# Optimization experiments

Measured on AMD Instinct MI355X. Metric: run time of the kernel, lower is better.

Reference implementation:

```python
import jax, jax.numpy as jnp
import numpy as np

CH = 512   # ch_in = c_out
P = 8
SD = 512
NG = CH // P          # n_groups = 64
CIG = CH // NG        # c_in per group = 8
DN = ('NCHW', 'OIHW', 'NCHW')


def setup_inputs() -> dict:
    key = jax.random.key(0)
    ks = jax.random.split(key, 8)
    N, H, W = 8, 128, 128
    return {
        "style_encoding": jax.random.normal(ks[0], (N, SD, 4, 4), jnp.float32),
        "predicted": jax.random.normal(ks[1], (N, CH, H, W), jnp.float32),
        "dw_w": jax.random.normal(ks[2], (CH * CIG, SD, 2, 2), jnp.float32) * 0.02,
        "dw_b": jnp.zeros((CH * CIG,), jnp.float32),
        "pk_w": jax.random.normal(ks[3], (CH * CIG, SD), jnp.float32) * 0.02,
        "pk_b": jnp.zeros((CH * CIG,), jnp.float32),
        "pb_w": jax.random.normal(ks[4], (CH, SD), jnp.float32) * 0.02,
        "pb_b": jnp.zeros((CH,), jnp.float32),
    }


def reference(style_encoding, predicted, dw_w, dw_b, pk_w, pk_b, pb_w, pb_b):
    N, ch, h, w = predicted.shape
    # --- KernelPredictor ---
    # depthwise kernels: 2x2 conv on 4x4 style -> 3x3 spatial kernels
    dw = jax.lax.conv_general_dilated(style_encoding, dw_w, (1, 1), 'VALID',
                                      dimension_numbers=DN)
    dw = dw + dw_b[None, :, None, None]
    depthwise = dw.reshape(N, CH, CIG, 3, 3)
    # avg-pool 4x4 -> (N, SD); 1x1 convs become matmuls
    s_pool = style_encoding.mean(axis=(2, 3))
    pw_kn = (s_pool @ pk_w.T + pk_b).reshape(N, CH, CH // NG)
    pw_bias = s_pool @ pb_w.T + pb_b  # (N, CH)
    # --- instance norm (calc_mean_std, unbiased var, eps=1e-5) ---
    mean = predicted.mean(axis=(2, 3), keepdims=True)
    std = jnp.sqrt(predicted.var(axis=(2, 3), keepdims=True, ddof=1) + 1e-5)
    x = (predicted - mean) / std
    # --- reflect pad + per-sample grouped convs, batched as groups ---
    x = jnp.pad(x, ((0, 0), (0, 0), (1, 1), (1, 1)), mode='reflect')
    xb = x.reshape(1, N * ch, h + 2, w + 2)
    wb = depthwise.reshape(N * CH, CIG, 3, 3)
    depth = jax.lax.conv_general_dilated(xb, wb, (1, 1), 'VALID',
                                         dimension_numbers=DN,
                                         feature_group_count=N * NG)
    wp = pw_kn.reshape(N * CH, CH // NG, 1, 1)
    out = jax.lax.conv_general_dilated(depth, wp, (1, 1), 'VALID',
                                       dimension_numbers=DN,
                                       feature_group_count=N * NG)
    out = out + pw_bias.reshape(1, N * CH, 1, 1)
    return out.reshape(N, ch, h, w)
```

## Files before the change

### kernel.cpp

```cpp
#include <hip/hip_runtime.h>

#define N_    8
#define CH_   512
#define SD_   512
#define CIG_  8
#define NG_   64
#define H_    128
#define W_    128
#define HW_   16384
#define KDW   2048
#define NP_   72
#define OC_   4096

#define WS_B     0
#define WS_SPOOL (WS_B + NP_ * KDW)
#define WS_PWKN  (WS_SPOOL + N_ * SD_)
#define WS_PWB   (WS_PWKN + N_ * OC_)
#define WS_DW    (WS_PWB + N_ * CH_)
#define WS_E     (WS_DW + N_ * OC_ * 9)
#define WS_MEAN  (WS_E + N_ * OC_ * 9)
#define WS_RSTD  (WS_MEAN + N_ * CH_)

__global__ __launch_bounds__(256) void prep(const float* __restrict__ style,
                                            float* __restrict__ B,
                                            float* __restrict__ spool,
                                            float* __restrict__ dwacc) {
  const int idx = blockIdx.x * 256 + threadIdx.x;
  const int NB = NP_ * KDW;
  const int NS = N_ * SD_;
  const int NZ = N_ * OC_ * 9;
  if (idx < NB) {
    const int np = idx >> 11;
    const int k = idx & 2047;
    const int n = np / 9, p = np % 9;
    const int py = p / 3, px = p % 3;
    const int ci = k >> 2, uv = k & 3;
    const int u = uv >> 1, v = uv & 1;
    B[idx] = style[(n * SD_ + ci) * 16 + (py + u) * 4 + (px + v)];
  } else if (idx < NB + NS) {
    const int j = idx - NB;
    const float* s = style + j * 16;
    float a = 0.f;
#pragma unroll
    for (int t = 0; t < 16; t++) a += s[t];
    spool[j] = a * (1.0f / 16.0f);
  } else if (idx < NB + NS + NZ) {
    dwacc[idx - NB - NS] = 0.0f;
  }
}

__global__ __launch_bounds__(256) void stats(const float* __restrict__ pred,
                                             float* __restrict__ meanv,
                                             float* __restrict__ rstdv) {
  const int nc = blockIdx.x;
  const float4* p = (const float4*)(pred + (size_t)nc * HW_);
  float s = 0.f, s2 = 0.f;
#pragma unroll
  for (int i = 0; i < 16; i++) {
    const float4 v = p[threadIdx.x + 256 * i];
    s += v.x + v.y + v.z + v.w;
    s2 += v.x * v.x + v.y * v.y + v.z * v.z + v.w * v.w;
  }
  for (int off = 32; off > 0; off >>= 1) {
    s += __shfl_down(s, off, 64);
    s2 += __shfl_down(s2, off, 64);
  }
  __shared__ float as[4], as2[4];
  const int wv = threadIdx.x >> 6;
  if ((threadIdx.x & 63) == 0) { as[wv] = s; as2[wv] = s2; }
  __syncthreads();
  if (threadIdx.x == 0) {
    const float S = as[0] + as[1] + as[2] + as[3];
    const float S2 = as2[0] + as2[1] + as2[2] + as2[3];
    const float mean = S * (1.0f / HW_);
    const float var = (S2 - S * mean) * (1.0f / (HW_ - 1));
    meanv[nc] = mean;
    rstdv[nc] = 1.0f / sqrtf(var + 1e-5f);
  }
}

__global__ __launch_bounds__(256) void pw_gemm(const float* __restrict__ spool,
                                               const float* __restrict__ pkw,
                                               const float* __restrict__ pkb,
                                               const float* __restrict__ pbw,
                                               const float* __restrict__ pbb,
                                               float* __restrict__ pwkn,
                                               float* __restrict__ pwbias) {
  __shared__ float sp[N_ * SD_];
  for (int i = threadIdx.x; i < N_ * SD_; i += 256) sp[i] = spool[i];
  __syncthreads();
  const int col = blockIdx.x * 256 + threadIdx.x;
  const float* w;
  float bias;
  if (col < OC_) { w = pkw + (size_t)col * SD_; bias = pkb[col]; }
  else           { w = pbw + (size_t)(col - OC_) * SD_; bias = pbb[col - OC_]; }
  float acc[8];
#pragma unroll
  for (int nn = 0; nn < 8; nn++) acc[nn] = 0.f;
  for (int k = 0; k < SD_; k += 4) {
    const float4 wv = *(const float4*)(w + k);
#pragma unroll
    for (int nn = 0; nn < 8; nn++) {
      const float4 sv = *(const float4*)(&sp[nn * SD_ + k]);
      acc[nn] = fmaf(wv.x, sv.x, acc[nn]);
      acc[nn] = fmaf(wv.y, sv.y, acc[nn]);
      acc[nn] = fmaf(wv.z, sv.z, acc[nn]);
      acc[nn] = fmaf(wv.w, sv.w, acc[nn]);
    }
  }
  if (col < OC_) {
#pragma unroll
    for (int nn = 0; nn < 8; nn++) pwkn[nn * OC_ + col] = acc[nn] + bias;
  } else {
#pragma unroll
    for (int nn = 0; nn < 8; nn++) pwbias[nn * CH_ + (col - OC_)] = acc[nn] + bias;
  }
}

__global__ __launch_bounds__(256) void dw_gemm(const float* __restrict__ Bg,
                                               const float* __restrict__ Wg,
                                               float* __restrict__ dwacc) {
  __shared__ float Wl[64 * 129];
  const int t = threadIdx.x;
  const int co0 = blockIdx.x * 128;
  const int kbase = blockIdx.y * 256;
  const int co = t & 127;
  const int npb = __builtin_amdgcn_readfirstlane((t >> 7) * 36);
  float acc[36];
#pragma unroll
  for (int j = 0; j < 36; j++) acc[j] = 0.f;

  for (int kc = 0; kc < 256; kc += 64) {
    __syncthreads();
    {
      const int kq = (t & 15) * 4;
      const int cob = t >> 4;
#pragma unroll
      for (int r = 0; r < 8; r++) {
        const int c = cob + r * 16;
        const float4 wv =
            *(const float4*)(Wg + (size_t)(co0 + c) * KDW + kbase + kc + kq);
        Wl[(kq + 0) * 129 + c] = wv.x;
        Wl[(kq + 1) * 129 + c] = wv.y;
        Wl[(kq + 2) * 129 + c] = wv.z;
        Wl[(kq + 3) * 129 + c] = wv.w;
      }
    }
    __syncthreads();
    const float* Bp = Bg + kbase + kc;
    for (int k = 0; k < 64; k += 4) {
      const float w0 = Wl[(k + 0) * 129 + co];
      const float w1 = Wl[(k + 1) * 129 + co];
      const float w2 = Wl[(k + 2) * 129 + co];
      const float w3 = Wl[(k + 3) * 129 + co];
#pragma unroll
      for (int j = 0; j < 36; j++) {
        const float4 b = *(const float4*)(Bp + (npb + j) * KDW + k);
        float a = acc[j];
        a = fmaf(w0, b.x, a);
        a = fmaf(w1, b.y, a);
        a = fmaf(w2, b.z, a);
        a = fmaf(w3, b.w, a);
        acc[j] = a;
      }
    }
  }
#pragma unroll
  for (int j = 0; j < 36; j++) {
    const int np = npb + j;
    const int n = np / 9, p = np % 9;
    atomicAdd(dwacc + (size_t)(n * OC_ + co0 + co) * 9 + p, acc[j]);
  }
}

__global__ __launch_bounds__(256) void eff_k(const float* __restrict__ dwacc,
                                             const float* __restrict__ dwb,
                                             const float* __restrict__ pwkn,
                                             float* __restrict__ Eg) {
  const int idx = blockIdx.x * 256 + threadIdx.x;
  const int co = idx & 7;
  int tmp = idx >> 3;
  const int p = tmp % 9;
  tmp /= 9;
  const int ci = tmp & 7;
  tmp >>= 3;
  const int gc = tmp & 63;
  const int n = tmp >> 6;
  const int c = gc * 8 + co;
  float a = 0.f;
#pragma unroll
  for (int j = 0; j < 8; j++) {
    const int ch = (gc * 8 + j) * 8 + ci;
    a = fmaf(pwkn[n * OC_ + c * 8 + j],
             dwacc[(size_t)(n * OC_ + ch) * 9 + p] + dwb[ch], a);
  }
  Eg[idx] = a;
}

#define ROWS 16
__global__ __launch_bounds__(256) void main_conv(const float* __restrict__ pred,
                                                 const float* __restrict__ Eg,
                                                 const float* __restrict__ pwb,
                                                 const float* __restrict__ meanv,
                                                 const float* __restrict__ rstdv,
                                                 float* __restrict__ out) {
  __shared__ float xl[8 * 18 * 132];
  __shared__ float El[8 * 9 * 8];
  __shared__ float cm[8], cr[8];
  const int t = threadIdx.x;
  const int yt = blockIdx.x;
  const int gc = blockIdx.y;
  const int n = blockIdx.z;
  const int chbase = n * CH_ + gc * 8;

  if (t < 8) {
    cm[t] = meanv[chbase + t];
    cr[t] = rstdv[chbase + t];
  }
  for (int i = t; i < 576; i += 256)
    El[i] = Eg[(size_t)(n * 64 + gc) * 576 + i];
  __syncthreads();

  const int y0 = yt * ROWS;
  for (int i = t; i < 8 * 18 * 130; i += 256) {
    const int col = i % 130;
    const int rr = (i / 130) % 18;
    const int ci = i / (130 * 18);
    int gy = y0 + rr - 1;
    gy = gy < 0 ? -gy : (gy > 127 ? 254 - gy : gy);
    int gx = col - 1;
    gx = gx < 0 ? -gx : (gx > 127 ? 254 - gx : gx);
    const float v = pred[((size_t)(chbase + ci) * 128 + gy) * 128 + gx];
    xl[(ci * 18 + rr) * 132 + col] = (v - cm[ci]) * cr[ci];
  }
  __syncthreads();

  const int y = t >> 4;
  const int xb = (t & 15) * 8;
  float acc[8][8];
#pragma unroll
  for (int co = 0; co < 8; co++)
#pragma unroll
    for (int px = 0; px < 8; px++) acc[co][px] = 0.f;

#pragma unroll 1
  for (int ci = 0; ci < 8; ci++) {
#pragma unroll
    for (int ky = 0; ky < 3; ky++) {
      const float* xr = &xl[(ci * 18 + y + ky) * 132 + xb];
      const float4 xa = *(const float4*)(xr);
      const float4 xc = *(const float4*)(xr + 4);
      const float xw[10] = {xa.x, xa.y, xa.z, xa.w, xc.x,
                            xc.y, xc.z, xc.w, xr[8], xr[9]};
#pragma unroll
      for (int kx = 0; kx < 3; kx++) {
        const float4 e0 = *(const float4*)(&El[(ci * 9 + ky * 3 + kx) * 8]);
        const float4 e1 = *(const float4*)(&El[(ci * 9 + ky * 3 + kx) * 8 + 4]);
        const float ev[8] = {e0.x, e0.y, e0.z, e0.w, e1.x, e1.y, e1.z, e1.w};
#pragma unroll
        for (int co = 0; co < 8; co++)
#pragma unroll
          for (int px = 0; px < 8; px++)
            acc[co][px] = fmaf(ev[co], xw[kx + px], acc[co][px]);
      }
    }
  }

  const int gy = y0 + y;
#pragma unroll
  for (int co = 0; co < 8; co++) {
    const float b = pwb[chbase + co];
    float* op = out + ((size_t)(chbase + co) * 128 + gy) * 128 + xb;
    float4 o0, o1;
    o0.x = acc[co][0] + b; o0.y = acc[co][1] + b;
    o0.z = acc[co][2] + b; o0.w = acc[co][3] + b;
    o1.x = acc[co][4] + b; o1.y = acc[co][5] + b;
    o1.z = acc[co][6] + b; o1.w = acc[co][7] + b;
    *(float4*)op = o0;
    *(float4*)(op + 4) = o1;
  }
}

extern "C" void kernel_launch(void* const* d_in, const int* in_sizes, int n_in,
                              void* d_out, int out_size, void* d_ws,
                              size_t ws_size, hipStream_t stream) {
  const float* style = (const float*)d_in[0];
  const float* pred = (const float*)d_in[1];
  const float* dww = (const float*)d_in[2];
  const float* dwb = (const float*)d_in[3];
  const float* pkw = (const float*)d_in[4];
  const float* pkb = (const float*)d_in[5];
  const float* pbw = (const float*)d_in[6];
  const float* pbb = (const float*)d_in[7];
  float* out = (float*)d_out;
  float* ws = (float*)d_ws;

  float* B = ws + WS_B;
  float* spool = ws + WS_SPOOL;
  float* pwkn = ws + WS_PWKN;
  float* pwbias = ws + WS_PWB;
  float* dwacc = ws + WS_DW;
  float* Eg = ws + WS_E;
  float* meanv = ws + WS_MEAN;
  float* rstdv = ws + WS_RSTD;

  prep<<<dim3(1744), dim3(256), 0, stream>>>(style, B, spool, dwacc);
  stats<<<dim3(4096), dim3(256), 0, stream>>>(pred, meanv, rstdv);
  pw_gemm<<<dim3(18), dim3(256), 0, stream>>>(spool, pkw, pkb, pbw, pbb, pwkn,
                                              pwbias);
  dw_gemm<<<dim3(32, 8), dim3(256), 0, stream>>>(B, dww, dwacc);
  eff_k<<<dim3(1152), dim3(256), 0, stream>>>(dwacc, dwb, pwkn, Eg);
  main_conv<<<dim3(8, 64, 8), dim3(256), 0, stream>>>(pred, Eg, pwbias, meanv,
                                                      rstdv, out);
}
```

Baseline: 975.5 us.

## Split-K small GEMMs with atomics and halve main_conv LDS tile for occupancy

The pw_gemm is split four ways along K, with results accumulated by atomicAdd into zeroed buffers, and the prep kernel is extended to zero those buffers. The dw_gemm split-K factor is doubled so more blocks run in parallel. main_conv now stages input channels in two halves of four, halving its shared-memory tile, and sets launch bounds to allow four blocks per CU, trading an extra barrier and reload phase for occupancy. Atomic accumulation makes the floating-point summation order nondeterministic.

```diff
diff --git a/kernel.cpp b/kernel.cpp
--- a/kernel.cpp
+++ b/kernel.cpp
@@ -21,14 +21,15 @@
 #define WS_MEAN  (WS_E + N_ * OC_ * 9)
 #define WS_RSTD  (WS_MEAN + N_ * CH_)
 
+#define NZERO (N_ * OC_ + N_ * CH_ + N_ * OC_ * 9)
+
 __global__ __launch_bounds__(256) void prep(const float* __restrict__ style,
                                             float* __restrict__ B,
                                             float* __restrict__ spool,
-                                            float* __restrict__ dwacc) {
+                                            float* __restrict__ zbase) {
   const int idx = blockIdx.x * 256 + threadIdx.x;
   const int NB = NP_ * KDW;
   const int NS = N_ * SD_;
-  const int NZ = N_ * OC_ * 9;
   if (idx < NB) {
     const int np = idx >> 11;
     const int k = idx & 2047;
@@ -44,8 +45,8 @@
 #pragma unroll
     for (int t = 0; t < 16; t++) a += s[t];
     spool[j] = a * (1.0f / 16.0f);
-  } else if (idx < NB + NS + NZ) {
-    dwacc[idx - NB - NS] = 0.0f;
+  } else if (idx < NB + NS + NZERO) {
+    zbase[idx - NB - NS] = 0.0f;
   }
 }
 
@@ -86,34 +87,41 @@
                                                const float* __restrict__ pbb,
                                                float* __restrict__ pwkn,
                                                float* __restrict__ pwbias) {
-  __shared__ float sp[N_ * SD_];
-  for (int i = threadIdx.x; i < N_ * SD_; i += 256) sp[i] = spool[i];
+  __shared__ float sp[N_ * 128];
+  const int kb = blockIdx.y * 128;
+  for (int i = threadIdx.x; i < N_ * 128; i += 256) {
+    const int nn = i >> 7, kk = i & 127;
+    sp[i] = spool[nn * SD_ + kb + kk];
+  }
   __syncthreads();
   const int col = blockIdx.x * 256 + threadIdx.x;
   const float* w;
   float bias;
-  if (col < OC_) { w = pkw + (size_t)col * SD_; bias = pkb[col]; }
-  else           { w = pbw + (size_t)(col - OC_) * SD_; bias = pbb[col - OC_]; }
+  if (col < OC_) { w = pkw + (size_t)col * SD_ + kb; bias = pkb[col]; }
+  else           { w = pbw + (size_t)(col - OC_) * SD_ + kb; bias = pbb[col - OC_]; }
   float acc[8];
 #pragma unroll
   for (int nn = 0; nn < 8; nn++) acc[nn] = 0.f;
-  for (int k = 0; k < SD_; k += 4) {
+  for (int k = 0; k < 128; k += 4) {
     const float4 wv = *(const float4*)(w + k);
 #pragma unroll
     for (int nn = 0; nn < 8; nn++) {
-      const float4 sv = *(const float4*)(&sp[nn * SD_ + k]);
+      const float4 sv = *(const float4*)(&sp[nn * 128 + k]);
       acc[nn] = fmaf(wv.x, sv.x, acc[nn]);
       acc[nn] = fmaf(wv.y, sv.y, acc[nn]);
       acc[nn] = fmaf(wv.z, sv.z, acc[nn]);
       acc[nn] = fmaf(wv.w, sv.w, acc[nn]);
     }
   }
+  const float badd = (blockIdx.y == 0) ? bias : 0.0f;
   if (col < OC_) {
 #pragma unroll
-    for (int nn = 0; nn < 8; nn++) pwkn[nn * OC_ + col] = acc[nn] + bias;
+    for (int nn = 0; nn < 8; nn++)
+      atomicAdd(&pwkn[nn * OC_ + col], acc[nn] + badd);
   } else {
 #pragma unroll
-    for (int nn = 0; nn < 8; nn++) pwbias[nn * CH_ + (col - OC_)] = acc[nn] + bias;
+    for (int nn = 0; nn < 8; nn++)
+      atomicAdd(&pwbias[nn * CH_ + (col - OC_)], acc[nn] + badd);
   }
 }
 
@@ -123,14 +131,14 @@
   __shared__ float Wl[64 * 129];
   const int t = threadIdx.x;
   const int co0 = blockIdx.x * 128;
-  const int kbase = blockIdx.y * 256;
+  const int kbase = blockIdx.y * 128;
   const int co = t & 127;
   const int npb = __builtin_amdgcn_readfirstlane((t >> 7) * 36);
   float acc[36];
 #pragma unroll
   for (int j = 0; j < 36; j++) acc[j] = 0.f;
 
-  for (int kc = 0; kc < 256; kc += 64) {
+  for (int kc = 0; kc < 128; kc += 64) {
     __syncthreads();
     {
       const int kq = (t & 15) * 4;
@@ -198,13 +206,11 @@
 }
 
 #define ROWS 16
-__global__ __launch_bounds__(256) void main_conv(const float* __restrict__ pred,
-                                                 const float* __restrict__ Eg,
-                                                 const float* __restrict__ pwb,
-                                                 const float* __restrict__ meanv,
-                                                 const float* __restrict__ rstdv,
-                                                 float* __restrict__ out) {
-  __shared__ float xl[8 * 18 * 132];
+__global__ __launch_bounds__(256, 4) void main_conv(
+    const float* __restrict__ pred, const float* __restrict__ Eg,
+    const float* __restrict__ pwb, const float* __restrict__ meanv,
+    const float* __restrict__ rstdv, float* __restrict__ out) {
+  __shared__ float xl[4 * 18 * 132];
   __shared__ float El[8 * 9 * 8];
   __shared__ float cm[8], cr[8];
   const int t = threadIdx.x;
@@ -222,19 +228,6 @@
   __syncthreads();
 
   const int y0 = yt * ROWS;
-  for (int i = t; i < 8 * 18 * 130; i += 256) {
-    const int col = i % 130;
-    const int rr = (i / 130) % 18;
-    const int ci = i / (130 * 18);
-    int gy = y0 + rr - 1;
-    gy = gy < 0 ? -gy : (gy > 127 ? 254 - gy : gy);
-    int gx = col - 1;
-    gx = gx < 0 ? -gx : (gx > 127 ? 254 - gx : gx);
-    const float v = pred[((size_t)(chbase + ci) * 128 + gy) * 128 + gx];
-    xl[(ci * 18 + rr) * 132 + col] = (v - cm[ci]) * cr[ci];
-  }
-  __syncthreads();
-
   const int y = t >> 4;
   const int xb = (t & 15) * 8;
   float acc[8][8];
@@ -244,24 +237,45 @@
     for (int px = 0; px < 8; px++) acc[co][px] = 0.f;
 
 #pragma unroll 1
-  for (int ci = 0; ci < 8; ci++) {
-#pragma unroll
-    for (int ky = 0; ky < 3; ky++) {
-      const float* xr = &xl[(ci * 18 + y + ky) * 132 + xb];
-      const float4 xa = *(const float4*)(xr);
-      const float4 xc = *(const float4*)(xr + 4);
-      const float xw[10] = {xa.x, xa.y, xa.z, xa.w, xc.x,
-                            xc.y, xc.z, xc.w, xr[8], xr[9]};
-#pragma unroll
-      for (int kx = 0; kx < 3; kx++) {
-        const float4 e0 = *(const float4*)(&El[(ci * 9 + ky * 3 + kx) * 8]);
-        const float4 e1 = *(const float4*)(&El[(ci * 9 + ky * 3 + kx) * 8 + 4]);
-        const float ev[8] = {e0.x, e0.y, e0.z, e0.w, e1.x, e1.y, e1.z, e1.w};
-#pragma unroll
-        for (int co = 0; co < 8; co++)
-#pragma unroll
-          for (int px = 0; px < 8; px++)
-            acc[co][px] = fmaf(ev[co], xw[kx + px], acc[co][px]);
+  for (int half = 0; half < 2; half++) {
+    if (half) __syncthreads();
+    for (int i = t; i < 4 * 18 * 130; i += 256) {
+      const int col = i % 130;
+      const int rr = (i / 130) % 18;
+      const int cl = i / (130 * 18);
+      const int ci = half * 4 + cl;
+      int gy = y0 + rr - 1;
+      gy = gy < 0 ? -gy : (gy > 127 ? 254 - gy : gy);
+      int gx = col - 1;
+      gx = gx < 0 ? -gx : (gx > 127 ? 254 - gx : gx);
+      const float v = pred[((size_t)(chbase + ci) * 128 + gy) * 128 + gx];
+      xl[(cl * 18 + rr) * 132 + col] = (v - cm[ci]) * cr[ci];
+    }
+    __syncthreads();
+
+#pragma unroll 1
+    for (int cl = 0; cl < 4; cl++) {
+      const int ci = half * 4 + cl;
+#pragma unroll
+      for (int ky = 0; ky < 3; ky++) {
+        const float* xr = &xl[(cl * 18 + y + ky) * 132 + xb];
+        const float4 xa = *(const float4*)(xr);
+        const float4 xc = *(const float4*)(xr + 4);
+        const float xw[10] = {xa.x, xa.y, xa.z, xa.w, xc.x,
+                              xc.y, xc.z, xc.w, xr[8], xr[9]};
+#pragma unroll
+        for (int kx = 0; kx < 3; kx++) {
+          const float4 e0 = *(const float4*)(&El[(ci * 9 + ky * 3 + kx) * 8]);
+          const float4 e1 =
+              *(const float4*)(&El[(ci * 9 + ky * 3 + kx) * 8 + 4]);
+          const float ev[8] = {e0.x, e0.y, e0.z, e0.w,
+                               e1.x, e1.y, e1.z, e1.w};
+#pragma unroll
+          for (int co = 0; co < 8; co++)
+#pragma unroll
+            for (int px = 0; px < 8; px++)
+              acc[co][px] = fmaf(ev[co], xw[kx + px], acc[co][px]);
+        }
       }
     }
   }
@@ -304,11 +318,11 @@
   float* meanv = ws + WS_MEAN;
   float* rstdv = ws + WS_RSTD;
 
-  prep<<<dim3(1744), dim3(256), 0, stream>>>(style, B, spool, dwacc);
+  prep<<<dim3(1888), dim3(256), 0, stream>>>(style, B, spool, pwkn);
   stats<<<dim3(4096), dim3(256), 0, stream>>>(pred, meanv, rstdv);
-  pw_gemm<<<dim3(18), dim3(256), 0, stream>>>(spool, pkw, pkb, pbw, pbb, pwkn,
-                                              pwbias);
-  dw_gemm<<<dim3(32, 8), dim3(256), 0, stream>>>(B, dww, dwacc);
+  pw_gemm<<<dim3(18, 4), dim3(256), 0, stream>>>(spool, pkw, pkb, pbw, pbb,
+                                                 pwkn, pwbias);
+  dw_gemm<<<dim3(32, 16), dim3(256), 0, stream>>>(B, dww, dwacc);
   eff_k<<<dim3(1152), dim3(256), 0, stream>>>(dwacc, dwb, pwkn, Eg);
   main_conv<<<dim3(8, 64, 8), dim3(256), 0, stream>>>(pred, Eg, pwbias, meanv,
                                                       rstdv, out);
```

After: 957.3 us. No clear change (-1.9%).
